# Kernel optimization log

Measured on AMD Instinct MI355X. Metric: run time of the kernel, lower is better.

Reference implementation:

```python
import jax, jax.numpy as jnp
import numpy as np

HIDDEN = 64
FORECAST = 30
B, T = 4096, 1024


def setup_inputs() -> dict:
    key = jax.random.key(0)
    ks = jax.random.split(key, 7)
    s = 1.0 / np.sqrt(HIDDEN)  # torch LSTM/Linear uniform init scale
    u = lambda k, shape: jax.random.uniform(k, shape, jnp.float32, -s, s)
    return {
        "x": jax.random.normal(ks[0], (B, T, 1), jnp.float32),
        "W_ih": u(ks[1], (4 * HIDDEN, 1)),      # gates order: i, f, g, o (torch)
        "W_hh": u(ks[2], (4 * HIDDEN, HIDDEN)),
        "b_ih": u(ks[3], (4 * HIDDEN,)),
        "b_hh": u(ks[4], (4 * HIDDEN,)),
        "fc_W": u(ks[5], (FORECAST, HIDDEN)),
        "fc_b": u(ks[6], (FORECAST,)),
    }


def _lstm_last_hidden(x, W_ih, W_hh, b_ih, b_hh):
    # Precompute input contributions for all timesteps: [B, T, 4H]
    xg = jnp.einsum("bti,gi->btg", x, W_ih) + b_ih + b_hh
    H = W_hh.shape[1]
    W_hh_T = W_hh.T  # [H, 4H]

    def step(carry, xt):  # xt: [B, 4H]
        h, c = carry
        gates = xt + h @ W_hh_T
        i, f, g, o = jnp.split(gates, 4, axis=-1)
        i = jax.nn.sigmoid(i)
        f = jax.nn.sigmoid(f)
        g = jnp.tanh(g)
        o = jax.nn.sigmoid(o)
        c = f * c + i * g
        h = o * jnp.tanh(c)
        return (h, c), None

    Bsz = x.shape[0]
    h0 = jnp.zeros((Bsz, H), x.dtype)
    c0 = jnp.zeros((Bsz, H), x.dtype)
    (h_last, _), _ = jax.lax.scan(step, (h0, c0), jnp.swapaxes(xg, 0, 1))
    return h_last  # [B, H]


def reference(x, W_ih, W_hh, b_ih, b_hh, fc_W, fc_b):
    h_last = _lstm_last_hidden(x, W_ih, W_hh, b_ih, b_hh)
    return h_last @ fc_W.T + fc_b  # [B, FORECAST]
```

## Files before the change

kernel.cpp:

```cpp
#include <hip/hip_runtime.h>
#include <math.h>

#define T_STEPS 1024
#define FORECAST 30

typedef __attribute__((ext_vector_type(8))) _Float16 half8;
typedef __attribute__((ext_vector_type(2))) _Float16 half2v;
typedef __attribute__((ext_vector_type(4))) float f32x4;
typedef __attribute__((ext_vector_type(2))) float f32x2;

__device__ __forceinline__ float rcp_fast(float v){ return __builtin_amdgcn_rcpf(v); }
__device__ __forceinline__ float exp2_fast(float v){ return __builtin_amdgcn_exp2f(v); }
__device__ __forceinline__ f32x4 mfma16(half8 a, half8 b, f32x4 c){
    return __builtin_amdgcn_mfma_f32_16x16x32_f16(a, b, c, 0, 0, 0);
}

__global__ __launch_bounds__(512, 1)
void lstm_mfma_kernel(const float* __restrict__ x,
                      const float* __restrict__ W_ih,
                      const float* __restrict__ W_hh,
                      const float* __restrict__ b_ih,
                      const float* __restrict__ b_hh,
                      const float* __restrict__ fc_W,
                      const float* __restrict__ fc_b,
                      float* __restrict__ out)
{
    __shared__ __align__(16) _Float16 hs[2][16][64];
    __shared__ float xs[2][64][16];

    const int tid = threadIdx.x;
    const int l   = tid & 63;
    const int w   = tid >> 6;
    const int l15 = l & 15;
    const int l4  = l >> 4;
    const int bb  = blockIdx.x * 16;

    const float L2E  = 1.44269504088896f;
    const float TL2E = 2.88539008177793f;

    const int   ga   = l15 & 3;
    const float Srow = (ga == 2) ? TL2E : -L2E;
    half8 A[2][2];
    #pragma unroll
    for (int T = 0; T < 2; ++T) {
        const int gc = ga*64 + w*8 + T*4 + (l15 >> 2);
        #pragma unroll
        for (int kc = 0; kc < 2; ++kc) {
            #pragma unroll
            for (int e = 0; e < 8; ++e) {
                const int p   = kc*32 + l4*8 + e;
                const int jin = (p & ~7) + ((p & 1) << 2) + ((p & 7) >> 1);
                A[T][kc][e] = (_Float16)(W_hh[gc*64 + jin] * Srow);
            }
        }
    }

    float wih[2][4], bia[2][4];
    #pragma unroll
    for (int T = 0; T < 2; ++T) {
        const int jT = w*8 + T*4 + l4;
        #pragma unroll
        for (int r = 0; r < 4; ++r) {
            const float S = (r == 2) ? TL2E : -L2E;
            const int   g = r*64 + jT;
            wih[T][r] = W_ih[g] * S;
            bia[T][r] = (b_ih[g] + b_hh[g]) * S;
        }
    }

    const int rbase = (l15*128 + l4*16) ^ ((l15&7)<<4);
    const int hwoff = (l15*128 + w*16 + l4*4) ^ ((l15&7)<<4);
    char* hbase = (char*)hs;

    #pragma unroll
    for (int it = 0; it < 2; ++it) {
        const int b = w*2 + it;
        xs[0][l][b] = x[(long long)(bb + b)*T_STEPS + l];
    }
    __syncthreads();

    f32x2 cc = {0.f, 0.f}, hh01 = {0.f, 0.f};
    float xv = xs[0][0][l15];

    for (int t = 0; t < T_STEPS; ++t) {
        half8 b0, b1;
        if (t > 0) {
            const char* hp = hbase + ((t + 1) & 1) * 2048;
            b0 = *(const half8*)(hp + rbase);
            b1 = *(const half8*)(hp + (rbase ^ 64));
        }

        if ((t & 63) == 0 && t + 64 < T_STEPS) {
            #pragma unroll
            for (int it = 0; it < 2; ++it) {
                const int b = w*2 + it;
                xs[(((t >> 6) & 1)) ^ 1][l][b] =
                    x[(long long)(bb + b)*T_STEPS + t + 64 + l];
            }
        }

        f32x4 acc0, acc1;
        #pragma unroll
        for (int r = 0; r < 4; ++r) {
            acc0[r] = fmaf(xv, wih[0][r], bia[0][r]);
            acc1[r] = fmaf(xv, wih[1][r], bia[1][r]);
        }

        if (t > 0) {
            acc0 = mfma16(A[0][0], b0, acc0);
            acc1 = mfma16(A[1][0], b0, acc1);
            acc0 = mfma16(A[0][1], b1, acc0);
            acc1 = mfma16(A[1][1], b1, acc1);
        }

        const int t1 = (t + 1 < T_STEPS) ? t + 1 : t;
        const float xvn = xs[(t1 >> 6) & 1][t1 & 63][l15];

        f32x2 eI, eF, eG, eO;
        eI[0] = exp2_fast(acc0[0]); eI[1] = exp2_fast(acc1[0]);
        eF[0] = exp2_fast(acc0[1]); eF[1] = exp2_fast(acc1[1]);
        eG[0] = exp2_fast(acc0[2]); eG[1] = exp2_fast(acc1[2]);
        eO[0] = exp2_fast(acc0[3]); eO[1] = exp2_fast(acc1[3]);
        const f32x2 u  = eI + 1.0f;
        const f32x2 v  = eF + 1.0f;
        const f32x2 s  = eG + 1.0f;
        const f32x2 m  = s - 2.0f;
        const f32x2 us = u * s;
        const f32x2 vm = v * m;
        const f32x2 N  = cc * us + vm;
        const f32x2 Dd = us * v;
        f32x2 rD; rD[0] = rcp_fast(Dd[0]); rD[1] = rcp_fast(Dd[1]);
        cc = N * rD;
        f32x2 a2 = cc * TL2E;
        a2[0] = fminf(a2[0], 80.f); a2[1] = fminf(a2[1], 80.f);
        f32x2 Tt; Tt[0] = exp2_fast(a2[0]); Tt[1] = exp2_fast(a2[1]);
        const f32x2 Dh = (eO + 1.0f) * (Tt + 1.0f);
        f32x2 rH; rH[0] = rcp_fast(Dh[0]); rH[1] = rcp_fast(Dh[1]);
        hh01 = (Tt - 1.0f) * rH;

        half2v hv;
        hv[0] = (_Float16)hh01[0];
        hv[1] = (_Float16)hh01[1];
        *(half2v*)(hbase + (t & 1)*2048 + hwoff) = hv;
        xv = xvn;
        __syncthreads();
    }

    float* hsc = (float*)xs;
    hsc[l15*64 + w*8 + l4]     = hh01[0];
    hsc[l15*64 + w*8 + 4 + l4] = hh01[1];
    __syncthreads();

    if (tid < 16*FORECAST) {
        const int b = tid / FORECAST;
        const int f = tid % FORECAST;
        float a = fc_b[f];
        #pragma unroll
        for (int jj = 0; jj < 64; ++jj)
            a = fmaf(hsc[b*64 + jj], fc_W[f*64 + jj], a);
        out[(long long)(bb + b)*FORECAST + f] = a;
    }
}

extern "C" void kernel_launch(void* const* d_in, const int* in_sizes, int n_in,
                              void* d_out, int out_size, void* d_ws, size_t ws_size,
                              hipStream_t stream) {
    const float* x    = (const float*)d_in[0];
    const float* W_ih = (const float*)d_in[1];
    const float* W_hh = (const float*)d_in[2];
    const float* b_ih = (const float*)d_in[3];
    const float* b_hh = (const float*)d_in[4];
    const float* fc_W = (const float*)d_in[5];
    const float* fc_b = (const float*)d_in[6];
    float* out = (float*)d_out;

    lstm_mfma_kernel<<<256, 512, 0, stream>>>(x, W_ih, W_hh, b_ih, b_hh, fc_W, fc_b, out);
}
```

Baseline: 396.6 us.

## Halve batch per block to run two LSTM blocks per CU with smaller barriers

Each block now handles 8 batch rows with 4 waves instead of 16 rows with 8 waves, and the grid doubles to 512 blocks so two blocks can share a CU (launch bounds 256,2). Each wave now owns 16 hidden units and issues 8 MFMAs per step. Lanes 8-15 of each MFMA tile carry duplicate batch columns, and a per-lane select picks the right tile results. The aim is to interleave two independent recurrences per CU and shrink the per-step barrier, at the cost of doubling MFMA work, half of it wasted, and raising register pressure.

```diff
diff --git a/kernel.cpp b/kernel.cpp
--- a/kernel.cpp
+++ b/kernel.cpp
@@ -3,6 +3,7 @@
 
 #define T_STEPS 1024
 #define FORECAST 30
+#define BPB 8
 
 typedef __attribute__((ext_vector_type(8))) _Float16 half8;
 typedef __attribute__((ext_vector_type(2))) _Float16 half2v;
@@ -15,7 +16,7 @@
     return __builtin_amdgcn_mfma_f32_16x16x32_f16(a, b, c, 0, 0, 0);
 }
 
-__global__ __launch_bounds__(512, 1)
+__global__ __launch_bounds__(256, 2)
 void lstm_mfma_kernel(const float* __restrict__ x,
                       const float* __restrict__ W_ih,
                       const float* __restrict__ W_hh,
@@ -25,40 +26,42 @@
                       const float* __restrict__ fc_b,
                       float* __restrict__ out)
 {
-    __shared__ __align__(16) _Float16 hs[2][16][64];
-    __shared__ float xs[2][64][16];
+    __shared__ __align__(16) _Float16 hs[2][BPB][64];
+    __shared__ float xs[2][64][BPB];
 
     const int tid = threadIdx.x;
     const int l   = tid & 63;
     const int w   = tid >> 6;
     const int l15 = l & 15;
     const int l4  = l >> 4;
-    const int bb  = blockIdx.x * 16;
+    const int b7  = l15 & 7;
+    const int T0  = (l15 >> 3) * 2;
+    const int bb  = blockIdx.x * BPB;
 
     const float L2E  = 1.44269504088896f;
     const float TL2E = 2.88539008177793f;
 
     const int   ga   = l15 & 3;
     const float Srow = (ga == 2) ? TL2E : -L2E;
-    half8 A[2][2];
+    half8 A[4][2];
     #pragma unroll
-    for (int T = 0; T < 2; ++T) {
-        const int gc = ga*64 + w*8 + T*4 + (l15 >> 2);
+    for (int T = 0; T < 4; ++T) {
+        const int gc = ga*64 + w*16 + T*4 + (l15 >> 2);
         #pragma unroll
         for (int kc = 0; kc < 2; ++kc) {
             #pragma unroll
             for (int e = 0; e < 8; ++e) {
                 const int p   = kc*32 + l4*8 + e;
-                const int jin = (p & ~7) + ((p & 1) << 2) + ((p & 7) >> 1);
+                const int jin = (p & ~15) + ((p & 3) << 2) + ((p >> 2) & 3);
                 A[T][kc][e] = (_Float16)(W_hh[gc*64 + jin] * Srow);
             }
         }
     }
 
-    float wih[2][4], bia[2][4];
+    float wih[4][4], bia[4][4];
     #pragma unroll
-    for (int T = 0; T < 2; ++T) {
-        const int jT = w*8 + T*4 + l4;
+    for (int T = 0; T < 4; ++T) {
+        const int jT = w*16 + T*4 + l4;
         #pragma unroll
         for (int r = 0; r < 4; ++r) {
             const float S = (r == 2) ? TL2E : -L2E;
@@ -68,8 +71,8 @@
         }
     }
 
-    const int rbase = (l15*128 + l4*16) ^ ((l15&7)<<4);
-    const int hwoff = (l15*128 + w*16 + l4*4) ^ ((l15&7)<<4);
+    const int rbase = (b7*128 + l4*16) ^ (b7<<4);
+    const int hwoff = (b7*128 + w*32 + l4*8 + T0*2) ^ (b7<<4);
     char* hbase = (char*)hs;
 
     #pragma unroll
@@ -80,14 +83,15 @@
     __syncthreads();
 
     f32x2 cc = {0.f, 0.f}, hh01 = {0.f, 0.f};
-    float xv = xs[0][0][l15];
+    float xv = xs[0][0][b7];
+    const bool lo = (l15 < 8);
 
     for (int t = 0; t < T_STEPS; ++t) {
-        half8 b0, b1;
+        half8 bf0, bf1;
         if (t > 0) {
-            const char* hp = hbase + ((t + 1) & 1) * 2048;
-            b0 = *(const half8*)(hp + rbase);
-            b1 = *(const half8*)(hp + (rbase ^ 64));
+            const char* hp = hbase + ((t + 1) & 1) * (BPB*128);
+            bf0 = *(const half8*)(hp + rbase);
+            bf1 = *(const half8*)(hp + (rbase ^ 64));
         }
 
         if ((t & 63) == 0 && t + 64 < T_STEPS) {
@@ -99,28 +103,36 @@
             }
         }
 
-        f32x4 acc0, acc1;
+        f32x4 acc[4];
+        #pragma unroll
+        for (int T = 0; T < 4; ++T)
+            #pragma unroll
+            for (int r = 0; r < 4; ++r)
+                acc[T][r] = fmaf(xv, wih[T][r], bia[T][r]);
+
+        if (t > 0) {
+            #pragma unroll
+            for (int T = 0; T < 4; ++T) {
+                acc[T] = mfma16(A[T][0], bf0, acc[T]);
+                acc[T] = mfma16(A[T][1], bf1, acc[T]);
+            }
+        }
+
+        f32x4 aA, aB;
         #pragma unroll
         for (int r = 0; r < 4; ++r) {
-            acc0[r] = fmaf(xv, wih[0][r], bia[0][r]);
-            acc1[r] = fmaf(xv, wih[1][r], bia[1][r]);
-        }
-
-        if (t > 0) {
-            acc0 = mfma16(A[0][0], b0, acc0);
-            acc1 = mfma16(A[1][0], b0, acc1);
-            acc0 = mfma16(A[0][1], b1, acc0);
-            acc1 = mfma16(A[1][1], b1, acc1);
+            aA[r] = lo ? acc[0][r] : acc[2][r];
+            aB[r] = lo ? acc[1][r] : acc[3][r];
         }
 
         const int t1 = (t + 1 < T_STEPS) ? t + 1 : t;
-        const float xvn = xs[(t1 >> 6) & 1][t1 & 63][l15];
+        const float xvn = xs[(t1 >> 6) & 1][t1 & 63][b7];
 
         f32x2 eI, eF, eG, eO;
-        eI[0] = exp2_fast(acc0[0]); eI[1] = exp2_fast(acc1[0]);
-        eF[0] = exp2_fast(acc0[1]); eF[1] = exp2_fast(acc1[1]);
-        eG[0] = exp2_fast(acc0[2]); eG[1] = exp2_fast(acc1[2]);
-        eO[0] = exp2_fast(acc0[3]); eO[1] = exp2_fast(acc1[3]);
+        eI[0] = exp2_fast(aA[0]); eI[1] = exp2_fast(aB[0]);
+        eF[0] = exp2_fast(aA[1]); eF[1] = exp2_fast(aB[1]);
+        eG[0] = exp2_fast(aA[2]); eG[1] = exp2_fast(aB[2]);
+        eO[0] = exp2_fast(aA[3]); eO[1] = exp2_fast(aB[3]);
         const f32x2 u  = eI + 1.0f;
         const f32x2 v  = eF + 1.0f;
         const f32x2 s  = eG + 1.0f;
@@ -141,17 +153,17 @@
         half2v hv;
         hv[0] = (_Float16)hh01[0];
         hv[1] = (_Float16)hh01[1];
-        *(half2v*)(hbase + (t & 1)*2048 + hwoff) = hv;
+        *(half2v*)(hbase + (t & 1)*(BPB*128) + hwoff) = hv;
         xv = xvn;
         __syncthreads();
     }
 
     float* hsc = (float*)xs;
-    hsc[l15*64 + w*8 + l4]     = hh01[0];
-    hsc[l15*64 + w*8 + 4 + l4] = hh01[1];
+    hsc[b7*64 + w*16 + T0*4 + l4]       = hh01[0];
+    hsc[b7*64 + w*16 + (T0+1)*4 + l4]   = hh01[1];
     __syncthreads();
 
-    if (tid < 16*FORECAST) {
+    if (tid < BPB*FORECAST) {
         const int b = tid / FORECAST;
         const int f = tid % FORECAST;
         float a = fc_b[f];
@@ -174,5 +186,5 @@
     const float* fc_b = (const float*)d_in[6];
     float* out = (float*)d_out;
 
-    lstm_mfma_kernel<<<256, 512, 0, stream>>>(x, W_ih, W_hh, b_ih, b_hh, fc_W, fc_b, out);
+    lstm_mfma_kernel<<<512, 256, 0, stream>>>(x, W_ih, W_hh, b_ih, b_hh, fc_W, fc_b, out);
 }
```

Measured after the change: 496.2 us. +25.1%, slower.

## Replace tanh(c) with clamped Padé approximant and split MFMA accumulation chains

Applied to the files above, without the earlier changes.

Replaces the exp2-based tanh of the cell state with a clamped rational (Padé 7/6) approximation folded into the output-gate reciprocal, which takes the transcendental off the serial per-step critical path. It also splits the two K-halves of the recurrent MFMA into independent accumulators so the dependent MFMA chain is shorter. The t>0 branches are removed by zero-initialising the h buffer, and the f16 conversion uses a packed round-toward-zero instruction. The tanh approximation and RTZ rounding slightly change numerics, with saturation beyond |c|≈4.6 handled by the clamp.

```diff
diff --git a/kernel.cpp b/kernel.cpp
--- a/kernel.cpp
+++ b/kernel.cpp
@@ -11,8 +11,12 @@
 
 __device__ __forceinline__ float rcp_fast(float v){ return __builtin_amdgcn_rcpf(v); }
 __device__ __forceinline__ float exp2_fast(float v){ return __builtin_amdgcn_exp2f(v); }
+__device__ __forceinline__ float med3(float a, float lo, float hi){ return __builtin_amdgcn_fmed3f(a, lo, hi); }
 __device__ __forceinline__ f32x4 mfma16(half8 a, half8 b, f32x4 c){
     return __builtin_amdgcn_mfma_f32_16x16x32_f16(a, b, c, 0, 0, 0);
+}
+__device__ __forceinline__ half2v pack_f16(float a, float b){
+    return __builtin_bit_cast(half2v, __builtin_amdgcn_cvt_pkrtz(a, b));
 }
 
 __global__ __launch_bounds__(512, 1)
@@ -77,18 +81,16 @@
         const int b = w*2 + it;
         xs[0][l][b] = x[(long long)(bb + b)*T_STEPS + l];
     }
+    ((unsigned*)hs)[512 + tid] = 0u;
     __syncthreads();
 
     f32x2 cc = {0.f, 0.f}, hh01 = {0.f, 0.f};
     float xv = xs[0][0][l15];
 
     for (int t = 0; t < T_STEPS; ++t) {
-        half8 b0, b1;
-        if (t > 0) {
-            const char* hp = hbase + ((t + 1) & 1) * 2048;
-            b0 = *(const half8*)(hp + rbase);
-            b1 = *(const half8*)(hp + (rbase ^ 64));
-        }
+        const char* hp = hbase + ((t + 1) & 1) * 2048;
+        const half8 b0 = *(const half8*)(hp + rbase);
+        const half8 b1 = *(const half8*)(hp + (rbase ^ 64));
 
         if ((t & 63) == 0 && t + 64 < T_STEPS) {
             #pragma unroll
@@ -99,28 +101,26 @@
             }
         }
 
-        f32x4 acc0, acc1;
+        f32x4 acc0, acc1, p0, p1;
         #pragma unroll
         for (int r = 0; r < 4; ++r) {
             acc0[r] = fmaf(xv, wih[0][r], bia[0][r]);
             acc1[r] = fmaf(xv, wih[1][r], bia[1][r]);
+            p0[r] = 0.f; p1[r] = 0.f;
         }
-
-        if (t > 0) {
-            acc0 = mfma16(A[0][0], b0, acc0);
-            acc1 = mfma16(A[1][0], b0, acc1);
-            acc0 = mfma16(A[0][1], b1, acc0);
-            acc1 = mfma16(A[1][1], b1, acc1);
-        }
+        acc0 = mfma16(A[0][0], b0, acc0);
+        acc1 = mfma16(A[1][0], b0, acc1);
+        p0   = mfma16(A[0][1], b1, p0);
+        p1   = mfma16(A[1][1], b1, p1);
 
         const int t1 = (t + 1 < T_STEPS) ? t + 1 : t;
         const float xvn = xs[(t1 >> 6) & 1][t1 & 63][l15];
 
         f32x2 eI, eF, eG, eO;
-        eI[0] = exp2_fast(acc0[0]); eI[1] = exp2_fast(acc1[0]);
-        eF[0] = exp2_fast(acc0[1]); eF[1] = exp2_fast(acc1[1]);
-        eG[0] = exp2_fast(acc0[2]); eG[1] = exp2_fast(acc1[2]);
-        eO[0] = exp2_fast(acc0[3]); eO[1] = exp2_fast(acc1[3]);
+        eI[0] = exp2_fast(acc0[0] + p0[0]); eI[1] = exp2_fast(acc1[0] + p1[0]);
+        eF[0] = exp2_fast(acc0[1] + p0[1]); eF[1] = exp2_fast(acc1[1] + p1[1]);
+        eG[0] = exp2_fast(acc0[2] + p0[2]); eG[1] = exp2_fast(acc1[2] + p1[2]);
+        eO[0] = exp2_fast(acc0[3] + p0[3]); eO[1] = exp2_fast(acc1[3] + p1[3]);
         const f32x2 u  = eI + 1.0f;
         const f32x2 v  = eF + 1.0f;
         const f32x2 s  = eG + 1.0f;
@@ -131,16 +131,20 @@
         const f32x2 Dd = us * v;
         f32x2 rD; rD[0] = rcp_fast(Dd[0]); rD[1] = rcp_fast(Dd[1]);
         cc = N * rD;
-        f32x2 a2 = cc * TL2E;
-        a2[0] = fminf(a2[0], 80.f); a2[1] = fminf(a2[1], 80.f);
-        f32x2 Tt; Tt[0] = exp2_fast(a2[0]); Tt[1] = exp2_fast(a2[1]);
-        const f32x2 Dh = (eO + 1.0f) * (Tt + 1.0f);
+
+        f32x2 ct; ct[0] = med3(cc[0], -4.6f, 4.6f); ct[1] = med3(cc[1], -4.6f, 4.6f);
+        const f32x2 z  = ct * ct;
+        f32x2 q = z * 21.0f + 1260.0f;
+        q = z * q + 10395.0f;
+        const f32x2 Pn = ct * q;
+        f32x2 r = z + 210.0f;
+        r = z * r + 4725.0f;
+        r = z * r + 10395.0f;
+        const f32x2 Dh = (eO + 1.0f) * r;
         f32x2 rH; rH[0] = rcp_fast(Dh[0]); rH[1] = rcp_fast(Dh[1]);
-        hh01 = (Tt - 1.0f) * rH;
+        hh01 = Pn * rH;
 
-        half2v hv;
-        hv[0] = (_Float16)hh01[0];
-        hv[1] = (_Float16)hh01[1];
+        const half2v hv = pack_f16(hh01[0], hh01[1]);
         *(half2v*)(hbase + (t & 1)*2048 + hwoff) = hv;
         xv = xvn;
         __syncthreads();
```

After: 413.0 us. +4.1%, slower.
